# Optimization experiments

Measured on AMD Instinct MI355X. Metric: run time of the kernel, lower is better.

The kernel has to match this reference:

```python
import jax, jax.numpy as jnp
import numpy as np

EPS = 1e-9

def setup_inputs() -> dict:
    key = jax.random.key(0)
    k1, k2 = jax.random.split(key)
    N, K, D = 65536, 512, 768
    return {
        "embeddings": jax.random.normal(k1, (N, D), dtype=jnp.float32),
        "cluster_centers": jax.random.normal(k2, (K, D), dtype=jnp.float32),
        "alpha": 1.0,
    }


def reference(embeddings, cluster_centers, alpha):
    # Student-t soft assignment (DEC): q_ik = (1 + ||x_i - c_k||^2 / alpha)^(-(alpha+1)/2), row-normalized.
    # Squared distance via expansion to avoid materializing the [N, K, D] broadcast:
    x_sq = jnp.sum(embeddings * embeddings, axis=1, keepdims=True)          # [N, 1]
    c_sq = jnp.sum(cluster_centers * cluster_centers, axis=1)               # [K]
    cross = jnp.einsum("nd,kd->nk", embeddings, cluster_centers)            # [N, K]
    norm_squared = jnp.maximum(x_sq - 2.0 * cross + c_sq[None, :], 0.0)     # [N, K]
    numerator = 1.0 / (1.0 + norm_squared / alpha)
    power = (alpha + 1.0) / 2.0
    numerator = numerator ** power
    cluster_p = numerator / jnp.sum(numerator, axis=1, keepdims=True)       # [N, K]
    return cluster_p
```

## Files before the change

### kernel.cpp

```cpp
#include <hip/hip_runtime.h>
#include <hip/hip_bf16.h>

#define D_DIM 768
#define K_CL  512
#define BM    64
#define BK    32
#define NSTEP 24

using f32x4 = __attribute__((ext_vector_type(4))) float;
using s16x8 = __attribute__((ext_vector_type(8))) short;
using u16x8 = __attribute__((ext_vector_type(8))) unsigned short;
using u16x4 = __attribute__((ext_vector_type(4))) unsigned short;
typedef unsigned int u32;

static __device__ __forceinline__ unsigned short f2bf(float f) {
    __hip_bfloat16 h = __float2bfloat16(f);
    unsigned short u;
    __builtin_memcpy(&u, &h, 2);
    return u;
}

static __device__ __forceinline__ void gload_lds16(const void* g, void* l) {
    __builtin_amdgcn_global_load_lds(
        (const __attribute__((address_space(1))) u32*)g,
        (__attribute__((address_space(3))) u32*)l, 16, 0, 0);
}

__global__ void prep_centers_kernel(const float* __restrict__ C,
                                    unsigned short* __restrict__ Cbws,
                                    float* __restrict__ csq) {
    const int r = blockIdx.x;
    const int l = threadIdx.x;
    const float* src = C + (size_t)r * D_DIM;
    float sq = 0.f;
#pragma unroll
    for (int jj = 0; jj < 2; ++jj) {
        const int j = l + jj * 64;
        if (j < 96) {
            const int t = j >> 2, s = j & 3;
            const int k0 = t * 32 + s * 8;
            f32x4 v0 = *reinterpret_cast<const f32x4*>(src + k0);
            f32x4 v1 = *reinterpret_cast<const f32x4*>(src + k0 + 4);
            u16x8 b;
            b[0] = f2bf(v0[0]); b[1] = f2bf(v0[1]); b[2] = f2bf(v0[2]); b[3] = f2bf(v0[3]);
            b[4] = f2bf(v1[0]); b[5] = f2bf(v1[1]); b[6] = f2bf(v1[2]); b[7] = f2bf(v1[3]);
            sq += v0[0]*v0[0] + v0[1]*v0[1] + v0[2]*v0[2] + v0[3]*v0[3]
                + v1[0]*v1[0] + v1[1]*v1[1] + v1[2]*v1[2] + v1[3]*v1[3];
            const int g = t * 2048 + r * 4 + (s ^ ((r >> 1) & 3));
            *reinterpret_cast<u16x8*>(Cbws + (size_t)g * 8) = b;
        }
    }
#pragma unroll
    for (int m = 1; m < 64; m <<= 1) sq += __shfl_xor(sq, m, 64);
    if (l == 0) csq[r] = sq;
}

__global__ __launch_bounds__(512, 4) void dec_main_kernel(
    const float* __restrict__ X,
    const unsigned short* __restrict__ Cbws,
    const float* __restrict__ csq,
    const float* __restrict__ alpha_ptr,
    float* __restrict__ out)
{
    __shared__ unsigned short Al[2][BM * BK];
    __shared__ unsigned short Bl[2][K_CL * BK];
    __shared__ float part[8][BM];
    __shared__ float xsql[BM];
    __shared__ float invl[BM];

    const int tid  = threadIdx.x;
    const int lane = tid & 63;
    const int wn   = tid >> 6;
    const int m0   = blockIdx.x * BM;

    const int arow  = tid >> 3;
    const int acol8 = tid & 7;
    const float* aptr = X + (size_t)(m0 + arow) * D_DIM + acol8 * 4;
    const int awbyte = arow * 64
                     + ((((acol8 >> 1) ^ ((arow >> 1) & 3))) << 4)
                     + (acol8 & 1) * 8;

    const int fr = lane & 15;
    const int fg = lane >> 4;
    int aoff[4], boff[4];
#pragma unroll
    for (int mf = 0; mf < 4; ++mf) {
        const int r = mf * 16 + fr;
        aoff[mf] = r * 64 + ((fg ^ ((r >> 1) & 3)) << 4);
    }
#pragma unroll
    for (int nf = 0; nf < 4; ++nf) {
        const int r = wn * 64 + nf * 16 + fr;
        boff[nf] = r * 64 + ((fg ^ ((r >> 1) & 3)) << 4);
    }

    f32x4 acc[4][4] = {};
    float sqp = 0.f;

    f32x4 areg = *reinterpret_cast<const f32x4*>(aptr);
    {
        const unsigned short* bs = Cbws + (size_t)tid * 8;
#pragma unroll
        for (int q = 0; q < 4; ++q)
            gload_lds16(bs + (size_t)q * 512 * 8,
                        (char*)&Bl[0][0] + ((size_t)q * 512 + tid) * 16);
    }
    {
        u16x4 ab;
        ab[0] = f2bf(areg[0]); ab[1] = f2bf(areg[1]);
        ab[2] = f2bf(areg[2]); ab[3] = f2bf(areg[3]);
        sqp += areg[0]*areg[0] + areg[1]*areg[1] + areg[2]*areg[2] + areg[3]*areg[3];
        *reinterpret_cast<u16x4*>((char*)&Al[0][0] + awbyte) = ab;
    }
    areg = *reinterpret_cast<const f32x4*>(aptr + BK);
    asm volatile("s_waitcnt vmcnt(1) lgkmcnt(0)" ::: "memory");
    __builtin_amdgcn_sched_barrier(0);
    __builtin_amdgcn_s_barrier();

#pragma unroll
    for (int t = 0; t < NSTEP; ++t) {
        const int buf = t & 1;
        if (t + 1 < NSTEP) {
            const unsigned short* bs = Cbws + (size_t)(t + 1) * 2048 * 8 + (size_t)tid * 8;
#pragma unroll
            for (int q = 0; q < 4; ++q)
                gload_lds16(bs + (size_t)q * 512 * 8,
                            (char*)&Bl[buf ^ 1][0] + ((size_t)q * 512 + tid) * 16);
        }
        {
            s16x8 afr[4];
#pragma unroll
            for (int mf = 0; mf < 4; ++mf)
                afr[mf] = *reinterpret_cast<const s16x8*>((const char*)&Al[buf][0] + aoff[mf]);
            __builtin_amdgcn_s_setprio(1);
#pragma unroll
            for (int nf = 0; nf < 4; ++nf) {
                s16x8 bfr = *reinterpret_cast<const s16x8*>((const char*)&Bl[buf][0] + boff[nf]);
#pragma unroll
                for (int mf = 0; mf < 4; ++mf)
                    acc[mf][nf] = __builtin_amdgcn_mfma_f32_16x16x32_bf16(
                        afr[mf], bfr, acc[mf][nf], 0, 0, 0);
            }
            __builtin_amdgcn_s_setprio(0);
        }
        if (t + 1 < NSTEP) {
            u16x4 ab;
            ab[0] = f2bf(areg[0]); ab[1] = f2bf(areg[1]);
            ab[2] = f2bf(areg[2]); ab[3] = f2bf(areg[3]);
            sqp += areg[0]*areg[0] + areg[1]*areg[1] + areg[2]*areg[2] + areg[3]*areg[3];
            *reinterpret_cast<u16x4*>((char*)&Al[buf ^ 1][0] + awbyte) = ab;
            if (t + 2 < NSTEP) {
                areg = *reinterpret_cast<const f32x4*>(aptr + (t + 2) * BK);
                asm volatile("s_waitcnt vmcnt(1) lgkmcnt(0)" ::: "memory");
            } else {
                asm volatile("s_waitcnt vmcnt(0) lgkmcnt(0)" ::: "memory");
            }
            __builtin_amdgcn_sched_barrier(0);
            __builtin_amdgcn_s_barrier();
        }
    }

    sqp += __shfl_xor(sqp, 1, 64);
    sqp += __shfl_xor(sqp, 2, 64);
    sqp += __shfl_xor(sqp, 4, 64);
    if ((tid & 7) == 0) xsql[arow] = sqp;
    __syncthreads();

    const float alpha     = alpha_ptr[0];
    const float inv_alpha = 1.0f / alpha;
    const float power     = 0.5f * (alpha + 1.0f);
    const bool  p1        = (power == 1.0f);

    float csqr[4];
#pragma unroll
    for (int nf = 0; nf < 4; ++nf)
        csqr[nf] = csq[wn * 64 + nf * 16 + fr];

#pragma unroll
    for (int mf = 0; mf < 4; ++mf) {
#pragma unroll
        for (int j = 0; j < 4; ++j) {
            const int rloc = mf * 16 + fg * 4 + j;
            const float xs = xsql[rloc];
            float rp = 0.f;
#pragma unroll
            for (int nf = 0; nf < 4; ++nf) {
                float d2 = xs + csqr[nf] - 2.0f * acc[mf][nf][j];
                d2 = fmaxf(d2, 0.0f);
                const float base = 1.0f + d2 * inv_alpha;
                const float nm = p1 ? (1.0f / base)
                                    : exp2f(-power * log2f(base));
                acc[mf][nf][j] = nm;
                rp += nm;
            }
#pragma unroll
            for (int m = 1; m < 16; m <<= 1) rp += __shfl_xor(rp, m, 64);
            if (fr == 0) part[wn][rloc] = rp;
        }
    }
    __syncthreads();
    if (tid < BM) {
        float s = 0.f;
#pragma unroll
        for (int w = 0; w < 8; ++w) s += part[w][tid];
        invl[tid] = 1.0f / s;
    }
    __syncthreads();

#pragma unroll
    for (int mf = 0; mf < 4; ++mf) {
#pragma unroll
        for (int j = 0; j < 4; ++j) {
            const int rloc = mf * 16 + fg * 4 + j;
            const float iv = invl[rloc];
            float* orow = out + (size_t)(m0 + rloc) * K_CL + wn * 64 + fr;
#pragma unroll
            for (int nf = 0; nf < 4; ++nf)
                orow[nf * 16] = acc[mf][nf][j] * iv;
        }
    }
}

extern "C" void kernel_launch(void* const* d_in, const int* in_sizes, int n_in,
                              void* d_out, int out_size, void* d_ws, size_t ws_size,
                              hipStream_t stream) {
    const float* X     = (const float*)d_in[0];
    const float* C     = (const float*)d_in[1];
    const float* alpha = (const float*)d_in[2];
    float* out = (float*)d_out;
    const int N = in_sizes[0] / D_DIM;

    unsigned short* Cbws = (unsigned short*)d_ws;
    float* csq = (float*)((char*)d_ws + (size_t)K_CL * D_DIM * sizeof(unsigned short));

    prep_centers_kernel<<<K_CL, 64, 0, stream>>>(C, Cbws, csq);
    dec_main_kernel<<<N / BM, 512, 0, stream>>>(X, Cbws, csq, alpha, out);
}
```

Baseline: 114.2 us.

## Load center fragments directly into registers instead of staging through LDS

Centers are pre-laid out in MFMA fragment order, so each wave loads its B operand fragments straight from global memory into registers. This removes the large B tile in shared memory and the global-to-LDS copies. Each wave reads only its own columns and nothing is shared through LDS, so reuse now depends on L2/L1. The lower LDS footprint may raise occupancy, but global load latency is now exposed within each step. The main loop is also no longer fully unrolled.

```diff
diff --git a/kernel.cpp b/kernel.cpp
--- a/kernel.cpp
+++ b/kernel.cpp
@@ -11,19 +11,12 @@
 using s16x8 = __attribute__((ext_vector_type(8))) short;
 using u16x8 = __attribute__((ext_vector_type(8))) unsigned short;
 using u16x4 = __attribute__((ext_vector_type(4))) unsigned short;
-typedef unsigned int u32;
 
 static __device__ __forceinline__ unsigned short f2bf(float f) {
     __hip_bfloat16 h = __float2bfloat16(f);
     unsigned short u;
     __builtin_memcpy(&u, &h, 2);
     return u;
-}
-
-static __device__ __forceinline__ void gload_lds16(const void* g, void* l) {
-    __builtin_amdgcn_global_load_lds(
-        (const __attribute__((address_space(1))) u32*)g,
-        (__attribute__((address_space(3))) u32*)l, 16, 0, 0);
 }
 
 __global__ void prep_centers_kernel(const float* __restrict__ C,
@@ -46,7 +39,8 @@
             b[4] = f2bf(v1[0]); b[5] = f2bf(v1[1]); b[6] = f2bf(v1[2]); b[7] = f2bf(v1[3]);
             sq += v0[0]*v0[0] + v0[1]*v0[1] + v0[2]*v0[2] + v0[3]*v0[3]
                 + v1[0]*v1[0] + v1[1]*v1[1] + v1[2]*v1[2] + v1[3]*v1[3];
-            const int g = t * 2048 + r * 4 + (s ^ ((r >> 1) & 3));
+            const int g = t * 2048 + (r >> 6) * 256 + ((r >> 4) & 3) * 64
+                        + s * 16 + (r & 15);
             *reinterpret_cast<u16x8*>(Cbws + (size_t)g * 8) = b;
         }
     }
@@ -63,7 +57,6 @@
     float* __restrict__ out)
 {
     __shared__ unsigned short Al[2][BM * BK];
-    __shared__ unsigned short Bl[2][K_CL * BK];
     __shared__ float part[8][BM];
     __shared__ float xsql[BM];
     __shared__ float invl[BM];
@@ -82,29 +75,18 @@
 
     const int fr = lane & 15;
     const int fg = lane >> 4;
-    int aoff[4], boff[4];
-#pragma unroll
-    for (int mf = 0; mf < 4; ++mf) {
-        const int r = mf * 16 + fr;
-        aoff[mf] = r * 64 + ((fg ^ ((r >> 1) & 3)) << 4);
-    }
-#pragma unroll
-    for (int nf = 0; nf < 4; ++nf) {
-        const int r = wn * 64 + nf * 16 + fr;
-        boff[nf] = r * 64 + ((fg ^ ((r >> 1) & 3)) << 4);
-    }
+    const int abase = fr * 64 + ((fg ^ ((fr >> 1) & 3)) << 4);
+
+    const unsigned short* bptr = Cbws + (size_t)(wn * 256 + lane) * 8;
 
     f32x4 acc[4][4] = {};
+    s16x8 bA[4];
     float sqp = 0.f;
 
     f32x4 areg = *reinterpret_cast<const f32x4*>(aptr);
-    {
-        const unsigned short* bs = Cbws + (size_t)tid * 8;
-#pragma unroll
-        for (int q = 0; q < 4; ++q)
-            gload_lds16(bs + (size_t)q * 512 * 8,
-                        (char*)&Bl[0][0] + ((size_t)q * 512 + tid) * 16);
-    }
+#pragma unroll
+    for (int nf = 0; nf < 4; ++nf)
+        bA[nf] = *reinterpret_cast<const s16x8*>(bptr + nf * 512);
     {
         u16x4 ab;
         ab[0] = f2bf(areg[0]); ab[1] = f2bf(areg[1]);
@@ -113,48 +95,40 @@
         *reinterpret_cast<u16x4*>((char*)&Al[0][0] + awbyte) = ab;
     }
     areg = *reinterpret_cast<const f32x4*>(aptr + BK);
-    asm volatile("s_waitcnt vmcnt(1) lgkmcnt(0)" ::: "memory");
+    asm volatile("s_waitcnt lgkmcnt(0)" ::: "memory");
     __builtin_amdgcn_sched_barrier(0);
     __builtin_amdgcn_s_barrier();
 
-#pragma unroll
     for (int t = 0; t < NSTEP; ++t) {
-        const int buf = t & 1;
-        if (t + 1 < NSTEP) {
-            const unsigned short* bs = Cbws + (size_t)(t + 1) * 2048 * 8 + (size_t)tid * 8;
-#pragma unroll
-            for (int q = 0; q < 4; ++q)
-                gload_lds16(bs + (size_t)q * 512 * 8,
-                            (char*)&Bl[buf ^ 1][0] + ((size_t)q * 512 + tid) * 16);
-        }
         {
+            const char* ab = (const char*)&Al[t & 1][0] + abase;
             s16x8 afr[4];
 #pragma unroll
             for (int mf = 0; mf < 4; ++mf)
-                afr[mf] = *reinterpret_cast<const s16x8*>((const char*)&Al[buf][0] + aoff[mf]);
+                afr[mf] = *reinterpret_cast<const s16x8*>(ab + mf * 1024);
             __builtin_amdgcn_s_setprio(1);
 #pragma unroll
             for (int nf = 0; nf < 4; ++nf) {
-                s16x8 bfr = *reinterpret_cast<const s16x8*>((const char*)&Bl[buf][0] + boff[nf]);
 #pragma unroll
                 for (int mf = 0; mf < 4; ++mf)
                     acc[mf][nf] = __builtin_amdgcn_mfma_f32_16x16x32_bf16(
-                        afr[mf], bfr, acc[mf][nf], 0, 0, 0);
+                        afr[mf], bA[nf], acc[mf][nf], 0, 0, 0);
             }
             __builtin_amdgcn_s_setprio(0);
         }
         if (t + 1 < NSTEP) {
+            const unsigned short* bp = bptr + (size_t)(t + 1) * 16384;
+#pragma unroll
+            for (int nf = 0; nf < 4; ++nf)
+                bA[nf] = *reinterpret_cast<const s16x8*>(bp + nf * 512);
             u16x4 ab;
             ab[0] = f2bf(areg[0]); ab[1] = f2bf(areg[1]);
             ab[2] = f2bf(areg[2]); ab[3] = f2bf(areg[3]);
             sqp += areg[0]*areg[0] + areg[1]*areg[1] + areg[2]*areg[2] + areg[3]*areg[3];
-            *reinterpret_cast<u16x4*>((char*)&Al[buf ^ 1][0] + awbyte) = ab;
-            if (t + 2 < NSTEP) {
+            *reinterpret_cast<u16x4*>((char*)&Al[(t + 1) & 1][0] + awbyte) = ab;
+            if (t + 2 < NSTEP)
                 areg = *reinterpret_cast<const f32x4*>(aptr + (t + 2) * BK);
-                asm volatile("s_waitcnt vmcnt(1) lgkmcnt(0)" ::: "memory");
-            } else {
-                asm volatile("s_waitcnt vmcnt(0) lgkmcnt(0)" ::: "memory");
-            }
+            asm volatile("s_waitcnt lgkmcnt(0)" ::: "memory");
             __builtin_amdgcn_sched_barrier(0);
             __builtin_amdgcn_s_barrier();
         }
```

After: 119.7 us. +4.8%, slower.

## Give each wave a private B slice loaded by its own DMA, waited per wave

Applied to the files above, without the earlier changes.

Each wave now loads only the 64 center rows it consumes into its own LDS slice, and waits on its own vmcnt instead of relying on the block barrier to publish other waves' B loads. This is meant to loosen the coupling between the B prefetch and the workgroup barrier. The main loop is no longer force-unrolled, and the epilogue is split into separate p==1 and general branches to avoid a per-element select. Risks: waiting on vmcnt(4) while A loads are also outstanding may make ordering fragile, and the rolled loop adds loop overhead.

```diff
diff --git a/kernel.cpp b/kernel.cpp
--- a/kernel.cpp
+++ b/kernel.cpp
@@ -63,7 +63,7 @@
     float* __restrict__ out)
 {
     __shared__ unsigned short Al[2][BM * BK];
-    __shared__ unsigned short Bl[2][K_CL * BK];
+    __shared__ unsigned short Bl[8 * 2 * 2048];
     __shared__ float part[8][BM];
     __shared__ float xsql[BM];
     __shared__ float invl[BM];
@@ -82,29 +82,37 @@
 
     const int fr = lane & 15;
     const int fg = lane >> 4;
-    int aoff[4], boff[4];
+    int aoff[4], boffb[4];
 #pragma unroll
     for (int mf = 0; mf < 4; ++mf) {
         const int r = mf * 16 + fr;
         aoff[mf] = r * 64 + ((fg ^ ((r >> 1) & 3)) << 4);
     }
+    const int bslice = wn * 8192;
 #pragma unroll
     for (int nf = 0; nf < 4; ++nf) {
-        const int r = wn * 64 + nf * 16 + fr;
-        boff[nf] = r * 64 + ((fg ^ ((r >> 1) & 3)) << 4);
+        const int lr = nf * 16 + fr;
+        boffb[nf] = bslice + lr * 64 + ((fg ^ ((lr >> 1) & 3)) << 4);
+    }
+
+    const unsigned short* bsrc = Cbws + (size_t)(wn * 256) * 8 + (size_t)lane * 8;
+    char* bdst = (char*)&Bl[0] + bslice + lane * 16;
+
+#define B_DMA(tt, buf_)                                                        \
+    {                                                                          \
+        const unsigned short* bs_ = bsrc + (size_t)(tt) * 16384;               \
+        char* bd_ = bdst + (buf_) * 4096;                                      \
+        gload_lds16(bs_,          bd_);                                        \
+        gload_lds16(bs_ + 512,    bd_ + 1024);                                 \
+        gload_lds16(bs_ + 1024,   bd_ + 2048);                                 \
+        gload_lds16(bs_ + 1536,   bd_ + 3072);                                 \
     }
 
     f32x4 acc[4][4] = {};
     float sqp = 0.f;
 
     f32x4 areg = *reinterpret_cast<const f32x4*>(aptr);
-    {
-        const unsigned short* bs = Cbws + (size_t)tid * 8;
-#pragma unroll
-        for (int q = 0; q < 4; ++q)
-            gload_lds16(bs + (size_t)q * 512 * 8,
-                        (char*)&Bl[0][0] + ((size_t)q * 512 + tid) * 16);
-    }
+    B_DMA(0, 0);
     {
         u16x4 ab;
         ab[0] = f2bf(areg[0]); ab[1] = f2bf(areg[1]);
@@ -113,20 +121,18 @@
         *reinterpret_cast<u16x4*>((char*)&Al[0][0] + awbyte) = ab;
     }
     areg = *reinterpret_cast<const f32x4*>(aptr + BK);
-    asm volatile("s_waitcnt vmcnt(1) lgkmcnt(0)" ::: "memory");
+    asm volatile("s_waitcnt lgkmcnt(0)" ::: "memory");
     __builtin_amdgcn_sched_barrier(0);
     __builtin_amdgcn_s_barrier();
 
-#pragma unroll
     for (int t = 0; t < NSTEP; ++t) {
         const int buf = t & 1;
-        if (t + 1 < NSTEP) {
-            const unsigned short* bs = Cbws + (size_t)(t + 1) * 2048 * 8 + (size_t)tid * 8;
-#pragma unroll
-            for (int q = 0; q < 4; ++q)
-                gload_lds16(bs + (size_t)q * 512 * 8,
-                            (char*)&Bl[buf ^ 1][0] + ((size_t)q * 512 + tid) * 16);
-        }
+        if (t + 1 < NSTEP) B_DMA(t + 1, buf ^ 1);
+        __builtin_amdgcn_sched_barrier(0);
+        if (t + 1 < NSTEP)
+            asm volatile("s_waitcnt vmcnt(4)" ::: "memory");
+        else
+            asm volatile("s_waitcnt vmcnt(0)" ::: "memory");
         {
             s16x8 afr[4];
 #pragma unroll
@@ -135,7 +141,8 @@
             __builtin_amdgcn_s_setprio(1);
 #pragma unroll
             for (int nf = 0; nf < 4; ++nf) {
-                s16x8 bfr = *reinterpret_cast<const s16x8*>((const char*)&Bl[buf][0] + boff[nf]);
+                s16x8 bfr = *reinterpret_cast<const s16x8*>(
+                    (const char*)&Bl[0] + buf * 4096 + boffb[nf]);
 #pragma unroll
                 for (int mf = 0; mf < 4; ++mf)
                     acc[mf][nf] = __builtin_amdgcn_mfma_f32_16x16x32_bf16(
@@ -149,16 +156,14 @@
             ab[2] = f2bf(areg[2]); ab[3] = f2bf(areg[3]);
             sqp += areg[0]*areg[0] + areg[1]*areg[1] + areg[2]*areg[2] + areg[3]*areg[3];
             *reinterpret_cast<u16x4*>((char*)&Al[buf ^ 1][0] + awbyte) = ab;
-            if (t + 2 < NSTEP) {
+            if (t + 2 < NSTEP)
                 areg = *reinterpret_cast<const f32x4*>(aptr + (t + 2) * BK);
-                asm volatile("s_waitcnt vmcnt(1) lgkmcnt(0)" ::: "memory");
-            } else {
-                asm volatile("s_waitcnt vmcnt(0) lgkmcnt(0)" ::: "memory");
-            }
+            asm volatile("s_waitcnt lgkmcnt(0)" ::: "memory");
             __builtin_amdgcn_sched_barrier(0);
             __builtin_amdgcn_s_barrier();
         }
     }
+#undef B_DMA
 
     sqp += __shfl_xor(sqp, 1, 64);
     sqp += __shfl_xor(sqp, 2, 64);
@@ -176,26 +181,48 @@
     for (int nf = 0; nf < 4; ++nf)
         csqr[nf] = csq[wn * 64 + nf * 16 + fr];
 
-#pragma unroll
-    for (int mf = 0; mf < 4; ++mf) {
-#pragma unroll
-        for (int j = 0; j < 4; ++j) {
-            const int rloc = mf * 16 + fg * 4 + j;
-            const float xs = xsql[rloc];
-            float rp = 0.f;
-#pragma unroll
-            for (int nf = 0; nf < 4; ++nf) {
-                float d2 = xs + csqr[nf] - 2.0f * acc[mf][nf][j];
-                d2 = fmaxf(d2, 0.0f);
-                const float base = 1.0f + d2 * inv_alpha;
-                const float nm = p1 ? (1.0f / base)
-                                    : exp2f(-power * log2f(base));
-                acc[mf][nf][j] = nm;
-                rp += nm;
+    if (p1) {
+#pragma unroll
+        for (int mf = 0; mf < 4; ++mf) {
+#pragma unroll
+            for (int j = 0; j < 4; ++j) {
+                const int rloc = mf * 16 + fg * 4 + j;
+                const float xs = xsql[rloc];
+                float rp = 0.f;
+#pragma unroll
+                for (int nf = 0; nf < 4; ++nf) {
+                    float d2 = xs + csqr[nf] - 2.0f * acc[mf][nf][j];
+                    d2 = fmaxf(d2, 0.0f);
+                    const float nm = 1.0f / (1.0f + d2 * inv_alpha);
+                    acc[mf][nf][j] = nm;
+                    rp += nm;
+                }
+#pragma unroll
+                for (int m = 1; m < 16; m <<= 1) rp += __shfl_xor(rp, m, 64);
+                if (fr == 0) part[wn][rloc] = rp;
             }
-#pragma unroll
-            for (int m = 1; m < 16; m <<= 1) rp += __shfl_xor(rp, m, 64);
-            if (fr == 0) part[wn][rloc] = rp;
+        }
+    } else {
+#pragma unroll
+        for (int mf = 0; mf < 4; ++mf) {
+#pragma unroll
+            for (int j = 0; j < 4; ++j) {
+                const int rloc = mf * 16 + fg * 4 + j;
+                const float xs = xsql[rloc];
+                float rp = 0.f;
+#pragma unroll
+                for (int nf = 0; nf < 4; ++nf) {
+                    float d2 = xs + csqr[nf] - 2.0f * acc[mf][nf][j];
+                    d2 = fmaxf(d2, 0.0f);
+                    const float base = 1.0f + d2 * inv_alpha;
+                    const float nm = exp2f(-power * log2f(base));
+                    acc[mf][nf][j] = nm;
+                    rp += nm;
+                }
+#pragma unroll
+                for (int m = 1; m < 16; m <<= 1) rp += __shfl_xor(rp, m, 64);
+                if (fr == 0) part[wn][rloc] = rp;
+            }
         }
     }
     __syncthreads();
```

Result: slower. 137.5 us (+20.4%).
